# Kernel optimization log

Measured on AMD Instinct MI355X. Metric: run time of the kernel, lower is better.

## Reference

```python
import jax, jax.numpy as jnp
import numpy as np

STRIDE = 16


def setup_inputs() -> dict:
    key = jax.random.key(0)
    kq, kk, kv, km = jax.random.split(key, 4)
    B, H, T, D = 2, 16, 2048, 64
    q = jax.random.normal(kq, (B, H, T, D), dtype=jnp.float32)
    k = jax.random.normal(kk, (B, H, T, D), dtype=jnp.float32)
    v = jax.random.normal(kv, (B, H, T, D), dtype=jnp.float32)
    mask = jax.random.randint(km, (B, 1, 1, T), 0, 2, dtype=jnp.int32)
    return {"q": q, "k": k, "v": v, "mask": mask}


def reference(q, k, v, mask):
    # q,k,v: (B,H,T,D); mask: (B,1,1,T_k)
    B, H, T_q, D = q.shape
    T_k = k.shape[2]
    scale = 1.0 / jnp.sqrt(jnp.float32(D))
    scores = jnp.einsum("bhqd,bhkd->bhqk", q, k) * scale
    rq = jnp.arange(T_q)[:, None]
    rk = jnp.arange(T_k)[None, :]
    stride_mask = (rk % STRIDE == 0) | (rq == rk)           # (T_q, T_k) bool
    NEG = jnp.float32(-1e9)
    scores = jnp.where(stride_mask[None, None], scores, NEG)
    scores = jnp.where(mask == 0, NEG, scores)
    attn = jax.nn.softmax(scores, axis=-1)
    out = jnp.einsum("bhqk,bhkd->bhqd", attn, v)
    return (out, attn)
```

## Files before the change

kernel.cpp:

```cpp
#include <hip/hip_runtime.h>
#include <hip/hip_bf16.h>

constexpr int B = 2, H = 16, T = 2048, D = 64;
constexpr int NS = T / 16;
constexpr int WAVES = 4, BLOCK = 256;
constexpr int CHUNKS = 16;
constexpr int ROWS_PER_BLOCK = T / CHUNKS;
constexpr int ROWS_PER_WAVE = ROWS_PER_BLOCK / WAVES;
constexpr int R = 4;
constexpr int GROUPS = ROWS_PER_WAVE / R;

__device__ __forceinline__ float rlf(float v, int l) {
    return __int_as_float(__builtin_amdgcn_readlane(__float_as_int(v), l));
}

__global__ __launch_bounds__(BLOCK, 2)
void strided_attn_kernel(const float* __restrict__ q,
                         const float* __restrict__ k,
                         const float* __restrict__ v,
                         const int*   __restrict__ mask,
                         float* __restrict__ out,
                         float* __restrict__ attn)
{
    __shared__ float4 Ks4[NS][16];
    __shared__ float  Vs[NS * 64];
    __shared__ int    msk[NS];

    const int blk   = blockIdx.x;
    const int bh    = blk / CHUNKS;
    const int chunk = blk % CHUNKS;
    const int b     = bh / H;

    const float* qb = q + (size_t)bh * T * D;
    const float* kb = k + (size_t)bh * T * D;
    const float* vb = v + (size_t)bh * T * D;
    const int*   mb = mask + (size_t)b * T;

    const int tid = threadIdx.x;

    for (int i = tid; i < NS * 16; i += BLOCK) {
        const int j = i >> 4, c = i & 15;
        Ks4[j][c ^ (j & 15)] =
            *reinterpret_cast<const float4*>(kb + (size_t)(j * 16) * D + c * 4);
        *reinterpret_cast<float4*>(Vs + j * 64 + c * 4) =
            *reinterpret_cast<const float4*>(vb + (size_t)(j * 16) * D + c * 4);
    }
    if (tid < NS) msk[tid] = mb[tid * 16];

    const int wave = tid >> 6, lane = tid & 63;
    const int row0 = chunk * ROWS_PER_BLOCK + wave * ROWS_PER_WAVE;
    const int j0 = lane, j1 = lane + 64;
    const int xsw = lane & 15;
    const size_t bhT = (size_t)bh * T;

    const int mvals = (lane < ROWS_PER_WAVE) ? mb[row0 + lane] : 0;

    __syncthreads();

    const int m0 = msk[j0], m1 = msk[j1];

    #pragma unroll 1
    for (int g = 0; g < GROUPS; ++g) {
        const int grow = row0 + g * R;

        const float4 qv = *reinterpret_cast<const float4*>(qb + (size_t)grow * D + lane * 4);
        const float4 kg = *reinterpret_cast<const float4*>(kb + (size_t)grow * D + lane * 4);
        float vdr[R];
        #pragma unroll
        for (int r = 0; r < R; ++r)
            vdr[r] = vb[(size_t)(grow + r) * D + lane];

        float ds = fmaf(qv.w, kg.w, fmaf(qv.z, kg.z, fmaf(qv.y, kg.y, qv.x * kg.x)));
        ds += __shfl_xor(ds, 1, 64);
        ds += __shfl_xor(ds, 2, 64);
        ds += __shfl_xor(ds, 4, 64);
        ds += __shfl_xor(ds, 8, 64);
        const float sdv = ds * 0.125f;

        float s0[R] = {0.f, 0.f, 0.f, 0.f};
        float s1[R] = {0.f, 0.f, 0.f, 0.f};
        #pragma unroll 4
        for (int cq = 0; cq < 16; ++cq) {
            const float4 k0  = Ks4[j0][cq ^ xsw];
            const float4 k1v = Ks4[j1][cq ^ xsw];
            #pragma unroll
            for (int r = 0; r < R; ++r) {
                const int src = 16 * r + cq;
                const float qx = rlf(qv.x, src);
                const float qy = rlf(qv.y, src);
                const float qz = rlf(qv.z, src);
                const float qw = rlf(qv.w, src);
                s0[r] = fmaf(qw, k0.w,  fmaf(qz, k0.z,  fmaf(qy, k0.y,  fmaf(qx, k0.x,  s0[r]))));
                s1[r] = fmaf(qw, k1v.w, fmaf(qz, k1v.z, fmaf(qy, k1v.y, fmaf(qx, k1v.x, s1[r]))));
            }
        }

        float p0[R], p1[R], pd[R];
        #pragma unroll
        for (int r = 0; r < R; ++r) {
            float a0 = s0[r] * 0.125f, a1 = s1[r] * 0.125f;
            if (m0 == 0) a0 = -1e9f;
            if (m1 == 0) a1 = -1e9f;

            float sd = rlf(sdv, 16 * r);
            if (__builtin_amdgcn_readlane(mvals, g * R + r) == 0) sd = -1e9f;
            const bool qmod = (((g * R + r) & 15) == 0);

            const float e0 = __expf(a0);
            const float e1 = __expf(a1);
            const float ed = qmod ? 0.f : __expf(sd);
            float sum = e0 + e1;
            #pragma unroll
            for (int s = 32; s > 0; s >>= 1) sum += __shfl_xor(sum, s, 64);
            sum += ed;
            const float inv = 1.f / sum;

            p0[r] = e0 * inv;
            p1[r] = e1 * inv;
            pd[r] = ed * inv;
        }

        float acc[R];
        #pragma unroll
        for (int r = 0; r < R; ++r)
            acc[r] = pd[r] * vdr[r];

        #pragma unroll 8
        for (int j = 0; j < 64; ++j) {
            const float vj = Vs[j * 64 + lane];
            #pragma unroll
            for (int r = 0; r < R; ++r)
                acc[r] = fmaf(rlf(p0[r], j), vj, acc[r]);
        }
        #pragma unroll 8
        for (int j = 0; j < 64; ++j) {
            const float vj = Vs[(j + 64) * 64 + lane];
            #pragma unroll
            for (int r = 0; r < R; ++r)
                acc[r] = fmaf(rlf(p1[r], j), vj, acc[r]);
        }

        #pragma unroll
        for (int r = 0; r < R; ++r)
            out[(bhT + grow + r) * D + lane] = acc[r];

        #pragma unroll 1
        for (int t = 0; t < 8; ++t) {
            const int f    = t * 64 + lane;
            const int idx2 = ((t & 3) * 16) + (lane >> 2);
            #pragma unroll
            for (int r = 0; r < R; ++r) {
                const int qrow = grow + r;
                const float psrc = (t < 4) ? p0[r] : p1[r];
                const float pg   = __shfl(psrc, idx2, 64);
                float4 val = make_float4(0.f, 0.f, 0.f, 0.f);
                if ((lane & 3) == 0) val.x = pg;
                const bool qmod = (((g * R + r) & 15) == 0);
                const int  fq   = qrow >> 2;
                if (!qmod && t == (fq >> 6) && lane == (fq & 63)) {
                    if      (r == 0) val.x = pd[r];
                    else if (r == 1) val.y = pd[r];
                    else if (r == 2) val.z = pd[r];
                    else             val.w = pd[r];
                }
                *reinterpret_cast<float4*>(attn + (bhT + qrow) * (size_t)T + 4 * f) = val;
            }
        }
    }
}

extern "C" void kernel_launch(void* const* d_in, const int* in_sizes, int n_in,
                              void* d_out, int out_size, void* d_ws, size_t ws_size,
                              hipStream_t stream) {
    const float* q    = (const float*)d_in[0];
    const float* k    = (const float*)d_in[1];
    const float* v    = (const float*)d_in[2];
    const int*   mask = (const int*)d_in[3];

    float* out  = (float*)d_out;
    float* attn = out + (size_t)B * H * T * D;

    dim3 grid(B * H * CHUNKS);
    dim3 block(BLOCK);
    hipLaunchKernelGGL(strided_attn_kernel, grid, block, 0, stream,
                       q, k, v, mask, out, attn);
}
```

Before: 148.6 us.

## Store strided K/V in LDS as bf16 and raise occupancy with more chunks

Converts the strided K and V rows to packed bf16 when staging into shared memory, halving LDS footprint and LDS read traffic in the score and PV loops. Doubles the number of row chunks per head and raises the launch-bounds block minimum so more blocks can be resident. This adds conversion work, repeats K/V staging across twice as many blocks, and reduces the precision of scores and outputs.

```diff
diff --git a/kernel.cpp b/kernel.cpp
--- a/kernel.cpp
+++ b/kernel.cpp
@@ -4,7 +4,7 @@
 constexpr int B = 2, H = 16, T = 2048, D = 64;
 constexpr int NS = T / 16;
 constexpr int WAVES = 4, BLOCK = 256;
-constexpr int CHUNKS = 16;
+constexpr int CHUNKS = 32;
 constexpr int ROWS_PER_BLOCK = T / CHUNKS;
 constexpr int ROWS_PER_WAVE = ROWS_PER_BLOCK / WAVES;
 constexpr int R = 4;
@@ -13,8 +13,14 @@
 __device__ __forceinline__ float rlf(float v, int l) {
     return __int_as_float(__builtin_amdgcn_readlane(__float_as_int(v), l));
 }
-
-__global__ __launch_bounds__(BLOCK, 2)
+__device__ __forceinline__ unsigned bf16rne(float f) {
+    unsigned x = __float_as_uint(f);
+    return (x + 0x7fffu + ((x >> 16) & 1u)) >> 16;
+}
+__device__ __forceinline__ float bflo(unsigned u) { return __uint_as_float(u << 16); }
+__device__ __forceinline__ float bfhi(unsigned u) { return __uint_as_float(u & 0xffff0000u); }
+
+__global__ __launch_bounds__(BLOCK, 4)
 void strided_attn_kernel(const float* __restrict__ q,
                          const float* __restrict__ k,
                          const float* __restrict__ v,
@@ -22,9 +28,9 @@
                          float* __restrict__ out,
                          float* __restrict__ attn)
 {
-    __shared__ float4 Ks4[NS][16];
-    __shared__ float  Vs[NS * 64];
-    __shared__ int    msk[NS];
+    __shared__ uint2    Ks2[NS][16];
+    __shared__ unsigned Vp[NS / 2][64];
+    __shared__ int      msk[NS];
 
     const int blk   = blockIdx.x;
     const int bh    = blk / CHUNKS;
@@ -40,10 +46,17 @@
 
     for (int i = tid; i < NS * 16; i += BLOCK) {
         const int j = i >> 4, c = i & 15;
-        Ks4[j][c ^ (j & 15)] =
-            *reinterpret_cast<const float4*>(kb + (size_t)(j * 16) * D + c * 4);
-        *reinterpret_cast<float4*>(Vs + j * 64 + c * 4) =
-            *reinterpret_cast<const float4*>(vb + (size_t)(j * 16) * D + c * 4);
+        const float4 kv = *reinterpret_cast<const float4*>(kb + (size_t)(j * 16) * D + c * 4);
+        uint2 pk;
+        pk.x = bf16rne(kv.x) | (bf16rne(kv.y) << 16);
+        pk.y = bf16rne(kv.z) | (bf16rne(kv.w) << 16);
+        Ks2[j][c ^ (j & 15)] = pk;
+    }
+    for (int i = tid; i < (NS / 2) * 64; i += BLOCK) {
+        const int j2 = i >> 6, d = i & 63;
+        const float f0 = vb[(size_t)(32 * j2) * D + d];
+        const float f1 = vb[(size_t)(32 * j2 + 16) * D + d];
+        Vp[j2][d] = bf16rne(f0) | (bf16rne(f1) << 16);
     }
     if (tid < NS) msk[tid] = mb[tid * 16];
 
@@ -81,8 +94,10 @@
         float s1[R] = {0.f, 0.f, 0.f, 0.f};
         #pragma unroll 4
         for (int cq = 0; cq < 16; ++cq) {
-            const float4 k0  = Ks4[j0][cq ^ xsw];
-            const float4 k1v = Ks4[j1][cq ^ xsw];
+            const uint2 a0 = Ks2[j0][cq ^ xsw];
+            const uint2 a1 = Ks2[j1][cq ^ xsw];
+            const float k0x = bflo(a0.x), k0y = bfhi(a0.x), k0z = bflo(a0.y), k0w = bfhi(a0.y);
+            const float k1x = bflo(a1.x), k1y = bfhi(a1.x), k1z = bflo(a1.y), k1w = bfhi(a1.y);
             #pragma unroll
             for (int r = 0; r < R; ++r) {
                 const int src = 16 * r + cq;
@@ -90,8 +105,8 @@
                 const float qy = rlf(qv.y, src);
                 const float qz = rlf(qv.z, src);
                 const float qw = rlf(qv.w, src);
-                s0[r] = fmaf(qw, k0.w,  fmaf(qz, k0.z,  fmaf(qy, k0.y,  fmaf(qx, k0.x,  s0[r]))));
-                s1[r] = fmaf(qw, k1v.w, fmaf(qz, k1v.z, fmaf(qy, k1v.y, fmaf(qx, k1v.x, s1[r]))));
+                s0[r] = fmaf(qw, k0w, fmaf(qz, k0z, fmaf(qy, k0y, fmaf(qx, k0x, s0[r]))));
+                s1[r] = fmaf(qw, k1w, fmaf(qz, k1z, fmaf(qy, k1y, fmaf(qx, k1x, s1[r]))));
             }
         }
 
@@ -126,18 +141,22 @@
             acc[r] = pd[r] * vdr[r];
 
         #pragma unroll 8
-        for (int j = 0; j < 64; ++j) {
-            const float vj = Vs[j * 64 + lane];
+        for (int j2 = 0; j2 < 32; ++j2) {
+            const unsigned u = Vp[j2][lane];
+            const float ve = bflo(u), vo = bfhi(u);
             #pragma unroll
             for (int r = 0; r < R; ++r)
-                acc[r] = fmaf(rlf(p0[r], j), vj, acc[r]);
+                acc[r] = fmaf(rlf(p0[r], 2 * j2 + 1), vo,
+                         fmaf(rlf(p0[r], 2 * j2), ve, acc[r]));
         }
         #pragma unroll 8
-        for (int j = 0; j < 64; ++j) {
-            const float vj = Vs[(j + 64) * 64 + lane];
+        for (int j2 = 32; j2 < 64; ++j2) {
+            const unsigned u = Vp[j2][lane];
+            const float ve = bflo(u), vo = bfhi(u);
             #pragma unroll
             for (int r = 0; r < R; ++r)
-                acc[r] = fmaf(rlf(p1[r], j), vj, acc[r]);
+                acc[r] = fmaf(rlf(p1[r], 2 * (j2 - 32) + 1), vo,
+                         fmaf(rlf(p1[r], 2 * (j2 - 32)), ve, acc[r]));
         }
 
         #pragma unroll
```

Result: faster. 145.3 us (-2.2%).
